# Kernel tuning notes

Hardware: AMD Instinct MI355X
Metric: run time of the kernel (lower is better)

The kernel has to match this reference:

```python
import jax, jax.numpy as jnp
import numpy as np
from jax import lax

B, Q, T, NC = 64, 256, 256, 256
COST_CLASS = 1.0
COST_BBOX = 1.0
MAX_DIST = 100.0
BIG = 1e9


def setup_inputs() -> dict:
    key = jax.random.key(0)
    k1, k2, k3, k4 = jax.random.split(key, 4)
    pos = jax.random.uniform(k1, (B, Q, 2), jnp.float32) * 200.0
    logits = jax.random.normal(k2, (B, Q, NC), jnp.float32)
    outputs = jnp.concatenate([pos, logits], axis=-1)  # [B,Q,2+NC]
    tgt_pos = jax.random.uniform(k3, (B, T, 2), jnp.float32) * 200.0
    tgt_ids = jax.random.randint(k4, (B, T), 0, NC, jnp.int32)
    return {"outputs": outputs, "tgt_pos": tgt_pos, "tgt_ids": tgt_ids}


def build_cost(outputs, tgt_pos, tgt_ids):
    # class distribution and position come from slices of the raw output tensor
    prob = jax.nn.softmax(outputs[..., 2:], axis=-1)  # [B,Q,NC]
    out_pos = outputs[..., :2]                        # [B,Q,2]
    # cost_class = -out_prob[:, tgt_ids] (per batch element, bs==1 in forward_)
    cost_class = -jax.vmap(lambda p, t: p[:, t])(prob, tgt_ids)  # [B,Q,T]
    # torch.cdist(out_bbox, tgt_bbox, p=2)
    d = jnp.sqrt(jnp.sum((out_pos[:, :, None, :] - tgt_pos[:, None, :, :]) ** 2, axis=-1))  # [B,Q,T]
    cost_bbox = jnp.minimum(d, MAX_DIST)                            # clamp > max_distance
    cost_bbox = jnp.where(tgt_ids[:, None, :] <= 0, MAX_DIST, cost_bbox)  # mask padded targets
    C = COST_BBOX * cost_bbox + COST_CLASS * cost_class             # [B,Q,T]
    return jnp.transpose(C, (0, 2, 1))                              # [B,T,Q]: rows=targets, cols=queries


def hungarian_square(cost):
    """Jonker-Volgenant shortest augmenting path (e-maxx variant) on a square
    [n,n] cost matrix. Returns col index assigned to each row (min total cost),
    equivalent to scipy.optimize.linear_sum_assignment up to tie-breaking."""
    n = cost.shape[0]
    NDUM = n  # dummy column used as the start of each augmenting path
    big = jnp.asarray(BIG, cost.dtype)

    def assign_row(carry, i):
        p, u, v = carry  # p[j]: row matched to col j (-1 free); u,v: potentials
        p = p.at[NDUM].set(i)
        minv = jnp.full(n + 1, big, cost.dtype)
        used = jnp.zeros(n + 1, bool)
        way = jnp.full(n + 1, NDUM, jnp.int32)

        def cond(st):
            j0, p, u, v, minv, used, way = st
            return p[j0] >= 0  # stop when we reach a free column

        def body(st):
            j0, p, u, v, minv, used, way = st
            used = used.at[j0].set(True)
            i0 = p[j0]
            cur = cost[i0] - u[i0] - v[:n]                    # reduced costs of row i0
            better = (cur < minv[:n]) & (~used[:n])
            minv = minv.at[:n].set(jnp.where(better, cur, minv[:n]))
            way = way.at[:n].set(jnp.where(better, j0, way[:n]))
            masked = jnp.where(used[:n], big, minv[:n])
            j1 = jnp.argmin(masked).astype(jnp.int32)
            delta = masked[j1]
            u = u.at[jnp.where(used, p, n)].add(jnp.where(used, delta, 0.0))
            v = jnp.where(used, v - delta, v)
            minv = jnp.where(used, minv, minv - delta)
            return (j1, p, u, v, minv, used, way)

        j0, p, u, v, minv, used, way = lax.while_loop(
            cond, body, (jnp.asarray(NDUM, jnp.int32), p, u, v, minv, used, way))

        def aug_cond(st):
            return st[0] != NDUM

        def aug_body(st):
            j0, p = st
            j1 = way[j0]
            return (j1, p.at[j0].set(p[j1]))

        _, p = lax.while_loop(aug_cond, aug_body, (j0, p))
        return (p, u, v), None

    p0 = jnp.full(n + 1, -1, jnp.int32)
    u0 = jnp.zeros(n + 1, cost.dtype)
    v0 = jnp.zeros(n + 1, cost.dtype)
    (p, _, _), _ = lax.scan(assign_row, (p0, u0, v0), jnp.arange(n, dtype=jnp.int32))
    # invert col->row into row->col
    return jnp.zeros(n, jnp.int32).at[p[:n]].set(jnp.arange(n, dtype=jnp.int32))


def reference(outputs, tgt_pos, tgt_ids):
    C = build_cost(outputs, tgt_pos, tgt_ids)       # [B,T,Q]
    cols = jax.vmap(hungarian_square)(C)            # [B,T] query index per target row
    rows = jnp.broadcast_to(jnp.arange(T, dtype=jnp.int32), (B, T))
    indices = jnp.stack([rows, cols], axis=0)       # [2,B,T], matches torch.cat(dim=1) layout
    return indices, C
```

## Files before the change

kernel.cpp:

```cpp
#include <hip/hip_runtime.h>
#include <hip/hip_bf16.h>

#define BB   64
#define QQ   256
#define TT   256
#define CD   258
#define NM   256
#define BIGF 1000000000.0f
#define LROWS 128

__global__ __launch_bounds__(256) void sm_stats(const float* __restrict__ outs,
                                                float* __restrict__ rmax,
                                                float* __restrict__ rsum) {
    int row = blockIdx.x;
    int tid = threadIdx.x;
    float x = outs[(size_t)row * CD + 2 + tid];

    __shared__ float sw[5];
    float m = x;
#pragma unroll
    for (int off = 32; off; off >>= 1) m = fmaxf(m, __shfl_down(m, off, 64));
    if ((tid & 63) == 0) sw[tid >> 6] = m;
    __syncthreads();
    if (tid == 0) sw[4] = fmaxf(fmaxf(sw[0], sw[1]), fmaxf(sw[2], sw[3]));
    __syncthreads();
    float mx = sw[4];

    float s = expf(x - mx);
#pragma unroll
    for (int off = 32; off; off >>= 1) s += __shfl_down(s, off, 64);
    __syncthreads();
    if ((tid & 63) == 0) sw[tid >> 6] = s;
    __syncthreads();
    if (tid == 0) {
        rmax[row] = mx;
        rsum[row] = sw[0] + sw[1] + sw[2] + sw[3];
    }
}

__global__ __launch_bounds__(256) void build_cost(const float* __restrict__ outs,
                                                  const float* __restrict__ tpos,
                                                  const int* __restrict__ tids,
                                                  const float* __restrict__ rmax,
                                                  const float* __restrict__ rsum,
                                                  float* __restrict__ C) {
    int bt = blockIdx.x;
    int b  = bt >> 8;
    int q  = threadIdx.x;

    int   id = tids[bt];
    float tx = tpos[2 * bt];
    float ty = tpos[2 * bt + 1];

    const float* orow = outs + (size_t)(b * QQ + q) * CD;
    float dx = orow[0] - tx;
    float dy = orow[1] - ty;
    float d  = sqrtf(dx * dx + dy * dy);
    float bbox = fminf(d, 100.0f);
    if (id <= 0) bbox = 100.0f;

    int   rq  = b * QQ + q;
    float cls = expf(orow[2 + id] - rmax[rq]) / rsum[rq];

    C[(size_t)bt * QQ + q] = bbox - cls;
}

template <int CTRL, int RM>
__device__ __forceinline__ float dppmin(float x) {
    int y = __builtin_amdgcn_update_dpp(__float_as_int(x), __float_as_int(x),
                                        CTRL, RM, 0xF, false);
    return fminf(x, __int_as_float(y));
}

__global__ __launch_bounds__(64) void jv_solve(const float* __restrict__ Call,
                                               float* __restrict__ outIdx) {
    const int b    = blockIdx.x;
    const int lane = threadIdx.x;
    const float* cost = Call + (size_t)b * NM * NM;

    __shared__ float u_s[NM + 1];
    __shared__ int   p_s[NM + 1];
    __shared__ int   way_s[NM];
    extern __shared__ float crow[];

#pragma unroll 4
    for (int r = 0; r < LROWS; ++r) {
        float4 x = *(const float4*)(cost + (size_t)r * NM + lane * 4);
        *(float4*)(crow + r * NM + lane * 4) = x;
    }

    for (int k = lane; k <= NM; k += 64) {
        u_s[k] = 0.0f;
        p_s[k] = -1;
        if (k < NM) way_s[k] = NM;
    }

    float v[4] = {0.0f, 0.0f, 0.0f, 0.0f};

    for (int i = 0; i < NM; ++i) {
        float4 cr;
        if (i < LROWS) cr = *(const float4*)(crow + i * NM + lane * 4);
        else           cr = *(const float4*)(cost + (size_t)i * NM + lane * 4);

        if (lane == 0) p_s[NM] = i;
        int   pj[4];
        float ureg[4];
#pragma unroll
        for (int s = 0; s < 4; ++s) {
            pj[s]   = p_s[lane * 4 + s];
            ureg[s] = (pj[s] >= 0) ? u_s[pj[s]] : 0.0f;
        }
        const float uof0 = ureg[0], uof1 = ureg[1], uof2 = ureg[2], uof3 = ureg[3];
        float minv[4] = {BIGF, BIGF, BIGF, BIGF};
        int   way[4]  = {NM, NM, NM, NM};
        unsigned usedm = 0;
        float ui = 0.0f;
        int   j0 = NM;
        float u0 = 0.0f;

        while (true) {
            if ((j0 >> 2) == lane) usedm |= 1u << (j0 & 3);

            float c4[4] = {cr.x, cr.y, cr.z, cr.w};
#pragma unroll
            for (int s = 0; s < 4; ++s) {
                float cur = c4[s] - u0 - v[s];
                bool  un  = !(usedm & (1u << s));
                if (un && cur < minv[s]) { minv[s] = cur; way[s] = j0; }
            }

            float cand[4];
#pragma unroll
            for (int s = 0; s < 4; ++s)
                cand[s] = (usedm & (1u << s)) ? BIGF : minv[s];
            float cA = cand[0]; int lsA = 0; int pA = pj[0]; float uA = uof0;
            if (cand[1] < cA) { cA = cand[1]; lsA = 1; pA = pj[1]; uA = uof1; }
            float cB = cand[2]; int lsB = 2; int pB = pj[2]; float uB = uof2;
            if (cand[3] < cB) { cB = cand[3]; lsB = 3; pB = pj[3]; uB = uof3; }
            if (cB < cA)      { cA = cB;      lsA = lsB; pA = pB;  uA = uB;  }

            float x = cA;
            x = dppmin<0x111, 0xF>(x);
            x = dppmin<0x112, 0xF>(x);
            x = dppmin<0x114, 0xF>(x);
            x = dppmin<0x118, 0xF>(x);
            x = dppmin<0x142, 0xA>(x);
            x = dppmin<0x143, 0xC>(x);
            float wv = __int_as_float(__builtin_amdgcn_readlane(__float_as_int(x), 63));

            unsigned long long mm = __ballot(cA == wv);
            int flane = __ffsll(mm) - 1;
            int   pk  = ((pA + 1) << 2) | lsA;
            int   wpk = __builtin_amdgcn_readlane(pk, flane);
            float u0n = __int_as_float(__builtin_amdgcn_readlane(__float_as_int(uA), flane));
            int   i0n = (wpk >> 2) - 1;
            int   j1  = flane * 4 + (wpk & 3);
            float delta = wv;

            if (i0n >= 0) {
                if (i0n < LROWS) cr = *(const float4*)(crow + i0n * NM + lane * 4);
                else             cr = *(const float4*)(cost + (size_t)i0n * NM + lane * 4);
            }

            ui += delta;
#pragma unroll
            for (int s = 0; s < 4; ++s) {
                if (usedm & (1u << s)) { v[s] -= delta; ureg[s] += delta; }
                else                   { minv[s] -= delta; }
            }
            j0 = j1;
            if (i0n < 0) break;
            u0 = u0n;
        }

#pragma unroll
        for (int s = 0; s < 4; ++s) {
            way_s[lane * 4 + s] = way[s];
            if (usedm & (1u << s)) u_s[pj[s]] = ureg[s];
        }
        if (lane == 0) {
            u_s[i] = ui;
            int jj = j0;
            while (jj != NM) {
                int j1w = way_s[jj];
                p_s[jj] = p_s[j1w];
                jj = j1w;
            }
        }
    }

#pragma unroll
    for (int s = 0; s < 4; ++s) {
        int j = lane * 4 + s;
        outIdx[b * TT + j] = (float)j;
        int r = p_s[j];
        outIdx[BB * TT + b * TT + r] = (float)j;
    }
}

extern "C" void kernel_launch(void* const* d_in, const int* in_sizes, int n_in,
                              void* d_out, int out_size, void* d_ws, size_t ws_size,
                              hipStream_t stream) {
    const float* outs = (const float*)d_in[0];
    const float* tpos = (const float*)d_in[1];
    const int*   tids = (const int*)d_in[2];

    float* out  = (float*)d_out;
    float* C    = out + 2 * BB * TT;
    float* rmax = (float*)d_ws;
    float* rsum = rmax + BB * QQ;

    hipLaunchKernelGGL(sm_stats,   dim3(BB * QQ), dim3(256), 0, stream, outs, rmax, rsum);
    hipLaunchKernelGGL(build_cost, dim3(BB * TT), dim3(256), 0, stream, outs, tpos, tids, rmax, rsum, C);
    hipLaunchKernelGGL(jv_solve,   dim3(BB),      dim3(64),
                       LROWS * NM * sizeof(float), stream, C, out);
}
```

Measured before the change: 2.534 ms.

## Carry argmin payload through DPP reduction and parallelize path augmentation

The wavefront min-reduction now carries a packed row/column payload alongside the value, which removes the ballot/ffs and dependent readlane steps on every Dijkstra iteration. Used columns get minv set to BIG instead of a separate candidate pass, and the branchy updates become selects. Augmentation walks the way[] chain held in registers via readlane, then applies the p updates in parallel across lanes from a shared path buffer instead of running a serial lane-0 loop through shared memory. More cost rows (152) are also cached in LDS. The parallel path update reads p_s values that other lanes may be writing in the same pass, and tie-breaking in the reduction may differ from before.

Measured after the change: 3.060 ms. 20.8% more time.

```diff
diff --git a/kernel.cpp b/kernel.cpp
--- a/kernel.cpp
+++ b/kernel.cpp
@@ -7,7 +7,7 @@
 #define CD   258
 #define NM   256
 #define BIGF 1000000000.0f
-#define LROWS 128
+#define LROWS 152
 
 __global__ __launch_bounds__(256) void sm_stats(const float* __restrict__ outs,
                                                 float* __restrict__ rmax,
@@ -65,11 +65,21 @@
     C[(size_t)bt * QQ + q] = bbox - cls;
 }
 
+__device__ __forceinline__ float sel4f(const float a[4], int s) {
+    float r = a[0];
+    r = (s == 1) ? a[1] : r;
+    r = (s == 2) ? a[2] : r;
+    r = (s == 3) ? a[3] : r;
+    return r;
+}
+
 template <int CTRL, int RM>
-__device__ __forceinline__ float dppmin(float x) {
-    int y = __builtin_amdgcn_update_dpp(__float_as_int(x), __float_as_int(x),
-                                        CTRL, RM, 0xF, false);
-    return fminf(x, __int_as_float(y));
+__device__ __forceinline__ void dppstep(float& x, int& p) {
+    float fy = __int_as_float(__builtin_amdgcn_update_dpp(
+        __float_as_int(x), __float_as_int(x), CTRL, RM, 0xF, false));
+    int   py = __builtin_amdgcn_update_dpp(p, p, CTRL, RM, 0xF, false);
+    p = (fy <= x) ? py : p;
+    x = fminf(x, fy);
 }
 
 __global__ __launch_bounds__(64) void jv_solve(const float* __restrict__ Call,
@@ -80,7 +90,7 @@
 
     __shared__ float u_s[NM + 1];
     __shared__ int   p_s[NM + 1];
-    __shared__ int   way_s[NM];
+    __shared__ int   path_s[NM + 1];
     extern __shared__ float crow[];
 
 #pragma unroll 4
@@ -88,11 +98,9 @@
         float4 x = *(const float4*)(cost + (size_t)r * NM + lane * 4);
         *(float4*)(crow + r * NM + lane * 4) = x;
     }
-
     for (int k = lane; k <= NM; k += 64) {
         u_s[k] = 0.0f;
         p_s[k] = -1;
-        if (k < NM) way_s[k] = NM;
     }
 
     float v[4] = {0.0f, 0.0f, 0.0f, 0.0f};
@@ -103,6 +111,7 @@
         else           cr = *(const float4*)(cost + (size_t)i * NM + lane * 4);
 
         if (lane == 0) p_s[NM] = i;
+
         int   pj[4];
         float ureg[4];
 #pragma unroll
@@ -110,7 +119,7 @@
             pj[s]   = p_s[lane * 4 + s];
             ureg[s] = (pj[s] >= 0) ? u_s[pj[s]] : 0.0f;
         }
-        const float uof0 = ureg[0], uof1 = ureg[1], uof2 = ureg[2], uof3 = ureg[3];
+        const float uof[4] = {ureg[0], ureg[1], ureg[2], ureg[3]};
         float minv[4] = {BIGF, BIGF, BIGF, BIGF};
         int   way[4]  = {NM, NM, NM, NM};
         unsigned usedm = 0;
@@ -119,54 +128,62 @@
         float u0 = 0.0f;
 
         while (true) {
-            if ((j0 >> 2) == lane) usedm |= 1u << (j0 & 3);
+            {
+                bool own = (j0 >> 2) == lane;
+                if (own) usedm |= 1u << (j0 & 3);
+#pragma unroll
+                for (int s = 0; s < 4; ++s) {
+                    bool mk = own && ((j0 & 3) == s);
+                    minv[s] = mk ? BIGF : minv[s];
+                }
+            }
 
             float c4[4] = {cr.x, cr.y, cr.z, cr.w};
 #pragma unroll
             for (int s = 0; s < 4; ++s) {
                 float cur = c4[s] - u0 - v[s];
                 bool  un  = !(usedm & (1u << s));
-                if (un && cur < minv[s]) { minv[s] = cur; way[s] = j0; }
-            }
-
-            float cand[4];
-#pragma unroll
-            for (int s = 0; s < 4; ++s)
-                cand[s] = (usedm & (1u << s)) ? BIGF : minv[s];
-            float cA = cand[0]; int lsA = 0; int pA = pj[0]; float uA = uof0;
-            if (cand[1] < cA) { cA = cand[1]; lsA = 1; pA = pj[1]; uA = uof1; }
-            float cB = cand[2]; int lsB = 2; int pB = pj[2]; float uB = uof2;
-            if (cand[3] < cB) { cB = cand[3]; lsB = 3; pB = pj[3]; uB = uof3; }
-            if (cB < cA)      { cA = cB;      lsA = lsB; pA = pB;  uA = uB;  }
-
-            float x = cA;
-            x = dppmin<0x111, 0xF>(x);
-            x = dppmin<0x112, 0xF>(x);
-            x = dppmin<0x114, 0xF>(x);
-            x = dppmin<0x118, 0xF>(x);
-            x = dppmin<0x142, 0xA>(x);
-            x = dppmin<0x143, 0xC>(x);
-            float wv = __int_as_float(__builtin_amdgcn_readlane(__float_as_int(x), 63));
-
-            unsigned long long mm = __ballot(cA == wv);
-            int flane = __ffsll(mm) - 1;
-            int   pk  = ((pA + 1) << 2) | lsA;
-            int   wpk = __builtin_amdgcn_readlane(pk, flane);
-            float u0n = __int_as_float(__builtin_amdgcn_readlane(__float_as_int(uA), flane));
-            int   i0n = (wpk >> 2) - 1;
-            int   j1  = flane * 4 + (wpk & 3);
-            float delta = wv;
+                bool  bt  = un && (cur < minv[s]);
+                minv[s] = bt ? cur : minv[s];
+                way[s]  = bt ? j0  : way[s];
+            }
+
+            float lv = fminf(fminf(minv[0], minv[1]), fminf(minv[2], minv[3]));
+            int ls  = (minv[0] == lv) ? 0 : (minv[1] == lv) ? 1
+                     : (minv[2] == lv) ? 2 : 3;
+            int pjs = (minv[0] == lv) ? pj[0] : (minv[1] == lv) ? pj[1]
+                     : (minv[2] == lv) ? pj[2] : pj[3];
+            int pay = ((pjs + 1) << 8) | (lane * 4 + ls);
+
+            float x = lv; int p = pay;
+            dppstep<0x111, 0xF>(x, p);
+            dppstep<0x112, 0xF>(x, p);
+            dppstep<0x114, 0xF>(x, p);
+            dppstep<0x118, 0xF>(x, p);
+            dppstep<0x142, 0xA>(x, p);
+            dppstep<0x143, 0xC>(x, p);
+
+            int   w     = __builtin_amdgcn_readlane(p, 63);
+            float delta = __int_as_float(
+                __builtin_amdgcn_readlane(__float_as_int(x), 63));
+            int i0n = (w >> 8) - 1;
+            int j1  = w & 255;
 
             if (i0n >= 0) {
                 if (i0n < LROWS) cr = *(const float4*)(crow + i0n * NM + lane * 4);
                 else             cr = *(const float4*)(cost + (size_t)i0n * NM + lane * 4);
             }
+            float usel = sel4f(uof, j1 & 3);
+            float u0n  = __int_as_float(__builtin_amdgcn_readlane(
+                __float_as_int(usel), j1 >> 2));
 
             ui += delta;
 #pragma unroll
             for (int s = 0; s < 4; ++s) {
-                if (usedm & (1u << s)) { v[s] -= delta; ureg[s] += delta; }
-                else                   { minv[s] -= delta; }
+                bool us = (usedm >> s) & 1;
+                v[s]    = us ? (v[s] - delta)    : v[s];
+                ureg[s] = us ? (ureg[s] + delta) : ureg[s];
+                minv[s] = us ? minv[s] : (minv[s] - delta);
             }
             j0 = j1;
             if (i0n < 0) break;
@@ -174,17 +191,30 @@
         }
 
 #pragma unroll
-        for (int s = 0; s < 4; ++s) {
-            way_s[lane * 4 + s] = way[s];
+        for (int s = 0; s < 4; ++s)
             if (usedm & (1u << s)) u_s[pj[s]] = ureg[s];
-        }
-        if (lane == 0) {
-            u_s[i] = ui;
-            int jj = j0;
-            while (jj != NM) {
-                int j1w = way_s[jj];
-                p_s[jj] = p_s[j1w];
-                jj = j1w;
+        if (lane == 0) u_s[i] = ui;
+
+        unsigned wlo = (unsigned)way[0] | ((unsigned)way[1] << 16);
+        unsigned whi = (unsigned)way[2] | ((unsigned)way[3] << 16);
+        int jj = j0, m = 0;
+        while (jj != NM) {
+            if (lane == 0) path_s[m] = jj;
+            int l  = jj >> 2;
+            int lo = __builtin_amdgcn_readlane((int)wlo, l);
+            int hi = __builtin_amdgcn_readlane((int)whi, l);
+            int wd = (jj & 2) ? hi : lo;
+            jj = (jj & 1) ? ((wd >> 16) & 0xffff) : (wd & 0xffff);
+            ++m;
+        }
+        if (lane == 0) path_s[m] = NM;
+
+        for (int base = 0; base < m; base += 64) {
+            int k = base + lane;
+            if (k < m) {
+                int nd = path_s[k];
+                int pv = p_s[path_s[k + 1]];
+                p_s[nd] = pv;
             }
         }
     }
```

## Walk augmenting path via readlane and parallelize p updates; cache more rows

Applied to the files above, without the earlier changes.

Replaces the serial lane-0 augmentation walk through shared-memory way_s with a wave-wide walk that pulls way entries from registers with readlane, records the path in shared memory, and then applies the p updates in parallel across lanes. This avoids the per-row LDS store of way and the dependent serial LDS-load chain. It also raises the number of cost rows cached in LDS from 128 to 152, cutting global reads at the cost of more shared memory. The parallel update reads p_s of the next path node while other lanes write p_s, which relies on the old values still being visible within the wave.

Result: slower. 2.823 ms (+11.4%).

```diff
diff --git a/kernel.cpp b/kernel.cpp
--- a/kernel.cpp
+++ b/kernel.cpp
@@ -7,7 +7,7 @@
 #define CD   258
 #define NM   256
 #define BIGF 1000000000.0f
-#define LROWS 128
+#define LROWS 152
 
 __global__ __launch_bounds__(256) void sm_stats(const float* __restrict__ outs,
                                                 float* __restrict__ rmax,
@@ -80,7 +80,7 @@
 
     __shared__ float u_s[NM + 1];
     __shared__ int   p_s[NM + 1];
-    __shared__ int   way_s[NM];
+    __shared__ int   path_s[NM + 1];
     extern __shared__ float crow[];
 
 #pragma unroll 4
@@ -88,11 +88,9 @@
         float4 x = *(const float4*)(cost + (size_t)r * NM + lane * 4);
         *(float4*)(crow + r * NM + lane * 4) = x;
     }
-
     for (int k = lane; k <= NM; k += 64) {
         u_s[k] = 0.0f;
         p_s[k] = -1;
-        if (k < NM) way_s[k] = NM;
     }
 
     float v[4] = {0.0f, 0.0f, 0.0f, 0.0f};
@@ -174,17 +172,30 @@
         }
 
 #pragma unroll
-        for (int s = 0; s < 4; ++s) {
-            way_s[lane * 4 + s] = way[s];
+        for (int s = 0; s < 4; ++s)
             if (usedm & (1u << s)) u_s[pj[s]] = ureg[s];
-        }
-        if (lane == 0) {
-            u_s[i] = ui;
-            int jj = j0;
-            while (jj != NM) {
-                int j1w = way_s[jj];
-                p_s[jj] = p_s[j1w];
-                jj = j1w;
+        if (lane == 0) u_s[i] = ui;
+
+        unsigned wlo = (unsigned)way[0] | ((unsigned)way[1] << 16);
+        unsigned whi = (unsigned)way[2] | ((unsigned)way[3] << 16);
+        int jj = j0, m = 0;
+        while (jj != NM) {
+            if (lane == 0) path_s[m] = jj;
+            int l  = jj >> 2;
+            int lo = __builtin_amdgcn_readlane((int)wlo, l);
+            int hi = __builtin_amdgcn_readlane((int)whi, l);
+            int wd = (jj & 2) ? hi : lo;
+            jj = (jj & 1) ? ((wd >> 16) & 0xffff) : (wd & 0xffff);
+            ++m;
+        }
+        if (lane == 0) path_s[m] = NM;
+
+        for (int base = 0; base < m; base += 64) {
+            int k = base + lane;
+            if (k < m) {
+                int nd = path_s[k];
+                int pv = p_s[path_s[k + 1]];
+                p_s[nd] = pv;
             }
         }
     }
```
